# Kernel tuning notes

Hardware: AMD Instinct MI355X
Metric: run time of the kernel (lower is better)

Reference implementation:

```python
import jax, jax.numpy as jnp
import numpy as np

N, L, D = 32, 4096, 768
H = 12
DH = D // H
MLP_DIM = 4 * D


def setup_inputs() -> dict:
    key = jax.random.key(0)
    ks = jax.random.split(key, 12)
    xavier = jax.nn.initializers.xavier_uniform()
    inp = {
        "x": jax.random.normal(ks[0], (N, L, D), jnp.float32),
        "probe": xavier(ks[1], (1, 1, D), jnp.float32),
        # MHA projections (flax DenseGeneral layout: (d, h, dh) / out (h, dh, d))
        "wq": xavier(ks[2], (D, H, DH), jnp.float32),
        "bq": jnp.zeros((H, DH), jnp.float32),
        "wk": xavier(ks[3], (D, H, DH), jnp.float32),
        "bk": jnp.zeros((H, DH), jnp.float32),
        "wv": xavier(ks[4], (D, H, DH), jnp.float32),
        "bv": jnp.zeros((H, DH), jnp.float32),
        "wo": xavier(ks[5], (H, DH, D), jnp.float32),
        "bo": jnp.zeros((D,), jnp.float32),
        # LayerNorm
        "ln_scale": jnp.ones((D,), jnp.float32),
        "ln_bias": jnp.zeros((D,), jnp.float32),
        # MLP block
        "w1": xavier(ks[6], (D, MLP_DIM), jnp.float32),
        "b1": jax.random.normal(ks[7], (MLP_DIM,), jnp.float32) * 1e-6,
        "w2": xavier(ks[8], (MLP_DIM, D), jnp.float32),
        "b2": jax.random.normal(ks[9], (D,), jnp.float32) * 1e-6,
    }
    return inp


def _layernorm(x, scale, bias, eps=1e-6):
    mu = jnp.mean(x, axis=-1, keepdims=True)
    var = jnp.mean(jnp.square(x - mu), axis=-1, keepdims=True)
    return (x - mu) * jax.lax.rsqrt(var + eps) * scale + bias


def reference(x, probe, wq, bq, wk, bk, wv, bv, wo, bo,
              ln_scale, ln_bias, w1, b1, w2, b2):
    n, l, d = x.shape
    q_in = jnp.broadcast_to(probe, (n, 1, d))          # tile probe over batch
    q = jnp.einsum('nqd,dhe->nqhe', q_in, wq) + bq     # [n,1,h,dh]
    k = jnp.einsum('nld,dhe->nlhe', x, wk) + bk        # [n,l,h,dh]
    v = jnp.einsum('nld,dhe->nlhe', x, wv) + bv
    q = q / jnp.sqrt(jnp.asarray(DH, q.dtype))
    logits = jnp.einsum('nqhe,nlhe->nhql', q, k)       # [n,h,1,l]
    attn = jax.nn.softmax(logits, axis=-1)
    o = jnp.einsum('nhql,nlhe->nqhe', attn, v)         # [n,1,h,dh]
    xa = jnp.einsum('nqhe,hed->nqd', o, wo) + bo       # attention output [n,1,d]
    y = _layernorm(xa, ln_scale, ln_bias)
    mlp = jnp.dot(jax.nn.gelu(jnp.dot(y, w1) + b1), w2) + b2
    out = xa + mlp
    return out[:, 0]                                   # [n,d]
```

## Files before the change

### kernel.cpp

```cpp
#include <hip/hip_runtime.h>
#include <math.h>

#define N_B 32
#define L_S 4096
#define D_M 768
#define H_N 12

#define ZO_QH    0
#define ZO_XBAR  1024
#define ZO_O     295936
#define ZO_XA    320512
#define ZO_H1P   345088
#define ZO_MACC  443392
#define ZERO_N   467968
#define NZ_QK    467968
#define NZ_QB    477184
#define NZ_ATTN  477248
#define NZ_Y     2050112
#define NZ_H1    2074688

__global__ __launch_bounds__(256) void qh_kernel(
    const float* __restrict__ probe, const float* __restrict__ wq,
    const float* __restrict__ bq, float* __restrict__ qh) {
    int i = blockIdx.x * 256 + threadIdx.x;
    int d0 = blockIdx.y * 48;
    float acc = 0.f;
    for (int dd = 0; dd < 48; ++dd)
        acc += probe[d0 + dd] * wq[(size_t)(d0 + dd) * 768 + i];
    acc *= 0.125f;
    if (blockIdx.y == 0) acc += 0.125f * bq[i];
    atomicAdd(&qh[i], acc);
}

__global__ __launch_bounds__(256) void qk_kernel(
    const float* __restrict__ qh, const float* __restrict__ wk,
    const float* __restrict__ bk, float* __restrict__ qk,
    float* __restrict__ qb) {
    int h = blockIdx.x, dt = blockIdx.y, t = threadIdx.x;
    int d = dt * 256 + t;
    const float4* wk4 = (const float4*)(wk + (size_t)d * 768 + h * 64);
    const float4* qh4 = (const float4*)(qh + h * 64);
    float acc = 0.f;
    #pragma unroll
    for (int e4 = 0; e4 < 16; ++e4) {
        float4 w = wk4[e4], q = qh4[e4];
        acc += w.x * q.x + w.y * q.y + w.z * q.z + w.w * q.w;
    }
    qk[h * 768 + d] = acc;
    if (dt == 0 && t < 64) {
        float v = qh[h * 64 + t] * bk[h * 64 + t];
        #pragma unroll
        for (int off = 32; off > 0; off >>= 1) v += __shfl_xor(v, off);
        if (t == 0) qb[h] = v;
    }
}

__global__ __launch_bounds__(256) void logits_kernel(
    const float* __restrict__ x, const float* __restrict__ qk,
    const float* __restrict__ qb, float* __restrict__ attn) {
    int r = blockIdx.x * 256 + threadIdx.x;
    int n = r >> 12, l = r & 4095;
    const float4* xr4 = (const float4*)(x + (size_t)r * 768);
    const float4* qk4 = (const float4*)qk;
    float p[12];
    #pragma unroll
    for (int h = 0; h < 12; ++h) p[h] = qb[h];
    for (int d4 = 0; d4 < 192; ++d4) {
        float4 xv = xr4[d4];
        #pragma unroll
        for (int h = 0; h < 12; ++h) {
            float4 qv = qk4[h * 192 + d4];
            p[h] += xv.x * qv.x + xv.y * qv.y + xv.z * qv.z + xv.w * qv.w;
        }
    }
    #pragma unroll
    for (int h = 0; h < 12; ++h)
        attn[((size_t)(n * 12 + h)) * 4096 + l] = p[h];
}

__global__ __launch_bounds__(256) void softmax_kernel(float* __restrict__ attn) {
    float* p = attn + (size_t)blockIdx.x * 4096;
    int tid = threadIdx.x;
    __shared__ float red[4];
    float v[16];
    #pragma unroll
    for (int k = 0; k < 16; ++k) v[k] = p[tid + 256 * k];
    float m = -1e30f;
    #pragma unroll
    for (int k = 0; k < 16; ++k) m = fmaxf(m, v[k]);
    #pragma unroll
    for (int off = 32; off > 0; off >>= 1) m = fmaxf(m, __shfl_xor(m, off));
    int wave = tid >> 6;
    if ((tid & 63) == 0) red[wave] = m;
    __syncthreads();
    m = fmaxf(fmaxf(red[0], red[1]), fmaxf(red[2], red[3]));
    float s = 0.f;
    #pragma unroll
    for (int k = 0; k < 16; ++k) { v[k] = expf(v[k] - m); s += v[k]; }
    #pragma unroll
    for (int off = 32; off > 0; off >>= 1) s += __shfl_xor(s, off);
    __syncthreads();
    if ((tid & 63) == 0) red[wave] = s;
    __syncthreads();
    s = red[0] + red[1] + red[2] + red[3];
    float inv = 1.f / s;
    #pragma unroll
    for (int k = 0; k < 16; ++k) p[tid + 256 * k] = v[k] * inv;
}

__global__ __launch_bounds__(256) void xbar_kernel(
    const float* __restrict__ x, const float* __restrict__ attn,
    float* __restrict__ xbar) {
    int lc = blockIdx.x, dt = blockIdx.y, n = blockIdx.z;
    __shared__ __align__(16) float at_s[512 * 16];
    int t = threadIdx.x;
    for (int i = t; i < 512 * 12; i += 256) {
        int h = i >> 9, l = i & 511;
        at_s[l * 16 + h] = attn[((size_t)(n * 12 + h)) * 4096 + lc * 512 + l];
    }
    __syncthreads();
    int lane = t & 63, w = t >> 6;
    int h0 = w * 3;
    const float4* x4 = (const float4*)x;
    size_t base = ((size_t)n * 4096 + lc * 512) * 192 + dt * 64 + lane;
    float4 a0 = {0, 0, 0, 0}, a1 = {0, 0, 0, 0}, a2 = {0, 0, 0, 0};
    for (int l = 0; l < 512; ++l) {
        float4 xv = x4[base + (size_t)l * 192];
        float w0 = at_s[l * 16 + h0];
        float w1 = at_s[l * 16 + h0 + 1];
        float w2 = at_s[l * 16 + h0 + 2];
        a0.x += w0 * xv.x; a0.y += w0 * xv.y; a0.z += w0 * xv.z; a0.w += w0 * xv.w;
        a1.x += w1 * xv.x; a1.y += w1 * xv.y; a1.z += w1 * xv.z; a1.w += w1 * xv.w;
        a2.x += w2 * xv.x; a2.y += w2 * xv.y; a2.z += w2 * xv.z; a2.w += w2 * xv.w;
    }
    int d = dt * 256 + lane * 4;
    float* b0 = xbar + ((size_t)(n * 12 + h0)) * 768 + d;
    float* b1 = xbar + ((size_t)(n * 12 + h0 + 1)) * 768 + d;
    float* b2 = xbar + ((size_t)(n * 12 + h0 + 2)) * 768 + d;
    atomicAdd(b0 + 0, a0.x); atomicAdd(b0 + 1, a0.y); atomicAdd(b0 + 2, a0.z); atomicAdd(b0 + 3, a0.w);
    atomicAdd(b1 + 0, a1.x); atomicAdd(b1 + 1, a1.y); atomicAdd(b1 + 2, a1.z); atomicAdd(b1 + 3, a1.w);
    atomicAdd(b2 + 0, a2.x); atomicAdd(b2 + 1, a2.y); atomicAdd(b2 + 2, a2.z); atomicAdd(b2 + 3, a2.w);
}

__global__ __launch_bounds__(256) void oproj_kernel(
    const float* __restrict__ xbar, const float* __restrict__ wv,
    const float* __restrict__ bv, float* __restrict__ o) {
    int h = blockIdx.x, kk = blockIdx.y, t = threadIdx.x;
    int d0 = kk * 96;
    __shared__ __align__(16) float wv_s[96 * 64];
    __shared__ __align__(16) float xb_s[96 * 32];
    for (int i = t; i < 96 * 64; i += 256) {
        int d = i >> 6, e = i & 63;
        wv_s[i] = wv[(size_t)(d0 + d) * 768 + h * 64 + e];
    }
    for (int i = t; i < 96 * 32; i += 256) {
        int d = i >> 5, nn = i & 31;
        xb_s[i] = xbar[((size_t)(nn * 12 + h)) * 768 + d0 + d];
    }
    __syncthreads();
    int e = t & 63, ng = t >> 6;
    float acc[8] = {0, 0, 0, 0, 0, 0, 0, 0};
    for (int d = 0; d < 96; ++d) {
        float wvv = wv_s[d * 64 + e];
        const float4* xb4 = (const float4*)&xb_s[d * 32 + ng * 8];
        float4 p0 = xb4[0], p1 = xb4[1];
        acc[0] += p0.x * wvv; acc[1] += p0.y * wvv; acc[2] += p0.z * wvv; acc[3] += p0.w * wvv;
        acc[4] += p1.x * wvv; acc[5] += p1.y * wvv; acc[6] += p1.z * wvv; acc[7] += p1.w * wvv;
    }
    float bvv = (kk == 0) ? bv[h * 64 + e] : 0.f;
    #pragma unroll
    for (int k = 0; k < 8; ++k)
        atomicAdd(&o[(size_t)(ng * 8 + k) * 768 + h * 64 + e], acc[k] + bvv);
}

__global__ __launch_bounds__(256) void xaproj_kernel(
    const float* __restrict__ o, const float* __restrict__ wo,
    const float* __restrict__ bo, float* __restrict__ xa) {
    int dt = blockIdx.x, kk = blockIdx.y, t = threadIdx.x;
    int i0 = kk * 96;
    __shared__ __align__(16) float o_s[96 * 32];
    for (int idx = t; idx < 96 * 32; idx += 256) {
        int i = idx >> 5, nn = idx & 31;
        o_s[idx] = o[(size_t)nn * 768 + i0 + i];
    }
    __syncthreads();
    int d = dt * 256 + t;
    float acc[32];
    #pragma unroll
    for (int nn = 0; nn < 32; ++nn) acc[nn] = 0.f;
    for (int i = 0; i < 96; ++i) {
        float w = wo[(size_t)(i0 + i) * 768 + d];
        const float4* o4 = (const float4*)&o_s[i * 32];
        #pragma unroll
        for (int q = 0; q < 8; ++q) {
            float4 f = o4[q];
            acc[q * 4 + 0] += f.x * w; acc[q * 4 + 1] += f.y * w;
            acc[q * 4 + 2] += f.z * w; acc[q * 4 + 3] += f.w * w;
        }
    }
    float bov = (kk == 0) ? bo[d] : 0.f;
    #pragma unroll
    for (int nn = 0; nn < 32; ++nn)
        atomicAdd(&xa[(size_t)nn * 768 + d], acc[nn] + bov);
}

__global__ __launch_bounds__(256) void ln_kernel(
    const float* __restrict__ xa, const float* __restrict__ ln_scale,
    const float* __restrict__ ln_bias, float* __restrict__ y) {
    int n = blockIdx.x, tid = threadIdx.x;
    __shared__ float xs[768];
    __shared__ float red[4];
    for (int i = tid; i < 768; i += 256) xs[i] = xa[(size_t)n * 768 + i];
    __syncthreads();
    float lsum = 0.f;
    for (int i = tid; i < 768; i += 256) lsum += xs[i];
    #pragma unroll
    for (int off = 32; off > 0; off >>= 1) lsum += __shfl_xor(lsum, off);
    int wave = tid >> 6;
    if ((tid & 63) == 0) red[wave] = lsum;
    __syncthreads();
    float mu = (red[0] + red[1] + red[2] + red[3]) * (1.f / 768.f);
    __syncthreads();
    float lsq = 0.f;
    for (int i = tid; i < 768; i += 256) { float c = xs[i] - mu; lsq += c * c; }
    #pragma unroll
    for (int off = 32; off > 0; off >>= 1) lsq += __shfl_xor(lsq, off);
    if ((tid & 63) == 0) red[wave] = lsq;
    __syncthreads();
    float var = (red[0] + red[1] + red[2] + red[3]) * (1.f / 768.f);
    float rs = rsqrtf(var + 1e-6f);
    for (int i = tid; i < 768; i += 256)
        y[(size_t)n * 768 + i] = (xs[i] - mu) * rs * ln_scale[i] + ln_bias[i];
}

__global__ __launch_bounds__(256) void mlp1_kernel(
    const float* __restrict__ y, const float* __restrict__ w1,
    float* __restrict__ h1p) {
    int jt = blockIdx.x, kk = blockIdx.y, t = threadIdx.x;
    int d0 = kk * 48;
    __shared__ __align__(16) float y_s[48 * 32];
    for (int idx = t; idx < 48 * 32; idx += 256) {
        int d = idx >> 5, nn = idx & 31;
        y_s[idx] = y[(size_t)nn * 768 + d0 + d];
    }
    __syncthreads();
    int j = jt * 256 + t;
    float acc[32];
    #pragma unroll
    for (int nn = 0; nn < 32; ++nn) acc[nn] = 0.f;
    for (int d = 0; d < 48; ++d) {
        float w = w1[(size_t)(d0 + d) * 3072 + j];
        const float4* y4 = (const float4*)&y_s[d * 32];
        #pragma unroll
        for (int q = 0; q < 8; ++q) {
            float4 f = y4[q];
            acc[q * 4 + 0] += f.x * w; acc[q * 4 + 1] += f.y * w;
            acc[q * 4 + 2] += f.z * w; acc[q * 4 + 3] += f.w * w;
        }
    }
    #pragma unroll
    for (int nn = 0; nn < 32; ++nn)
        atomicAdd(&h1p[(size_t)nn * 3072 + j], acc[nn]);
}

__global__ __launch_bounds__(256) void gelu_kernel(
    const float* __restrict__ h1p, const float* __restrict__ b1,
    float* __restrict__ h1) {
    int j = blockIdx.x * 256 + threadIdx.x;
    int n = blockIdx.y;
    float tv = h1p[(size_t)n * 3072 + j] + b1[j];
    float g = 0.5f * tv * (1.f + tanhf(0.7978845608028654f * (tv + 0.044715f * tv * tv * tv)));
    h1[(size_t)n * 3072 + j] = g;
}

__global__ __launch_bounds__(256) void mlp2_kernel(
    const float* __restrict__ h1, const float* __restrict__ w2,
    float* __restrict__ macc) {
    int dt = blockIdx.x, kk = blockIdx.y, t = threadIdx.x;
    int j0 = kk * 48;
    __shared__ __align__(16) float h_s[48 * 32];
    for (int idx = t; idx < 48 * 32; idx += 256) {
        int j = idx >> 5, nn = idx & 31;
        h_s[idx] = h1[(size_t)nn * 3072 + j0 + j];
    }
    __syncthreads();
    int d = dt * 256 + t;
    float acc[32];
    #pragma unroll
    for (int nn = 0; nn < 32; ++nn) acc[nn] = 0.f;
    for (int j = 0; j < 48; ++j) {
        float w = w2[(size_t)(j0 + j) * 768 + d];
        const float4* h4 = (const float4*)&h_s[j * 32];
        #pragma unroll
        for (int q = 0; q < 8; ++q) {
            float4 f = h4[q];
            acc[q * 4 + 0] += f.x * w; acc[q * 4 + 1] += f.y * w;
            acc[q * 4 + 2] += f.z * w; acc[q * 4 + 3] += f.w * w;
        }
    }
    #pragma unroll
    for (int nn = 0; nn < 32; ++nn)
        atomicAdd(&macc[(size_t)nn * 768 + d], acc[nn]);
}

__global__ __launch_bounds__(256) void final_kernel(
    const float* __restrict__ xa, const float* __restrict__ b2,
    const float* __restrict__ macc, float* __restrict__ out) {
    int n = blockIdx.x, t = threadIdx.x;
    for (int i = t; i < 768; i += 256)
        out[(size_t)n * 768 + i] = xa[(size_t)n * 768 + i] + b2[i] + macc[(size_t)n * 768 + i];
}

extern "C" void kernel_launch(void* const* d_in, const int* in_sizes, int n_in,
                              void* d_out, int out_size, void* d_ws, size_t ws_size,
                              hipStream_t stream) {
    const float* x        = (const float*)d_in[0];
    const float* probe    = (const float*)d_in[1];
    const float* wq       = (const float*)d_in[2];
    const float* bq       = (const float*)d_in[3];
    const float* wk       = (const float*)d_in[4];
    const float* bk       = (const float*)d_in[5];
    const float* wv       = (const float*)d_in[6];
    const float* bv       = (const float*)d_in[7];
    const float* wo       = (const float*)d_in[8];
    const float* bo       = (const float*)d_in[9];
    const float* ln_scale = (const float*)d_in[10];
    const float* ln_bias  = (const float*)d_in[11];
    const float* w1       = (const float*)d_in[12];
    const float* b1       = (const float*)d_in[13];
    const float* w2       = (const float*)d_in[14];
    const float* b2       = (const float*)d_in[15];
    float* out = (float*)d_out;
    float* ws  = (float*)d_ws;

    float* qh   = ws + ZO_QH;
    float* xbar = ws + ZO_XBAR;
    float* o    = ws + ZO_O;
    float* xa   = ws + ZO_XA;
    float* h1p  = ws + ZO_H1P;
    float* macc = ws + ZO_MACC;
    float* qk   = ws + NZ_QK;
    float* qb   = ws + NZ_QB;
    float* attn = ws + NZ_ATTN;
    float* y    = ws + NZ_Y;
    float* h1   = ws + NZ_H1;

    hipMemsetAsync(ws, 0, (size_t)ZERO_N * sizeof(float), stream);
    qh_kernel<<<dim3(3, 16), 256, 0, stream>>>(probe, wq, bq, qh);
    qk_kernel<<<dim3(12, 3), 256, 0, stream>>>(qh, wk, bk, qk, qb);
    logits_kernel<<<512, 256, 0, stream>>>(x, qk, qb, attn);
    softmax_kernel<<<N_B * H_N, 256, 0, stream>>>(attn);
    xbar_kernel<<<dim3(8, 3, 32), 256, 0, stream>>>(x, attn, xbar);
    oproj_kernel<<<dim3(12, 8), 256, 0, stream>>>(xbar, wv, bv, o);
    xaproj_kernel<<<dim3(3, 8), 256, 0, stream>>>(o, wo, bo, xa);
    ln_kernel<<<N_B, 256, 0, stream>>>(xa, ln_scale, ln_bias, y);
    mlp1_kernel<<<dim3(12, 16), 256, 0, stream>>>(y, w1, h1p);
    gelu_kernel<<<dim3(12, 32), 256, 0, stream>>>(h1p, b1, h1);
    mlp2_kernel<<<dim3(3, 64), 256, 0, stream>>>(h1, w2, macc);
    final_kernel<<<N_B, 256, 0, stream>>>(xa, b2, macc, out);
}
```

Measured before the change: 820.5 us.

## Coalesce logits via wave-per-row reduction, fuse q/k prep and GELU into neighbours

The logits kernel now assigns one wavefront to each pair of rows. Lanes read contiguous float4 chunks, with qk staged in shared memory, and DPP cross-lane sums replace the old thread-per-row strided access that read whole rows per thread. The two query-prep kernels are merged into one kernel that recomputes qh redundantly in each block. GELU is folded into the mlp2 input load, and xbar reads its attention weights as a float4. These changes target uncoalesced x reads and extra launches, at the cost of redundant qh work in 36 blocks and an extra GELU recompute for each dt block.

```diff
diff --git a/kernel.cpp b/kernel.cpp
--- a/kernel.cpp
+++ b/kernel.cpp
@@ -6,40 +6,48 @@
 #define D_M 768
 #define H_N 12
 
-#define ZO_QH    0
-#define ZO_XBAR  1024
-#define ZO_O     295936
-#define ZO_XA    320512
-#define ZO_H1P   345088
-#define ZO_MACC  443392
-#define ZERO_N   467968
-#define NZ_QK    467968
-#define NZ_QB    477184
-#define NZ_ATTN  477248
-#define NZ_Y     2050112
-#define NZ_H1    2074688
-
-__global__ __launch_bounds__(256) void qh_kernel(
+#define ZO_XBAR  0
+#define ZO_O     294912
+#define ZO_XA    319488
+#define ZO_H1P   344064
+#define ZO_MACC  442368
+#define ZERO_N   466944
+#define NZ_QK    466944
+#define NZ_QB    476160
+#define NZ_ATTN  476224
+#define NZ_Y     2049088
+
+#define DPP_ADD(v, ctrl, rmask) \
+  v += __int_as_float(__builtin_amdgcn_update_dpp(0, __float_as_int(v), ctrl, rmask, 0xf, false))
+
+__device__ __forceinline__ float wave_sum63(float v) {
+    DPP_ADD(v, 0x111, 0xf);
+    DPP_ADD(v, 0x112, 0xf);
+    DPP_ADD(v, 0x114, 0xf);
+    DPP_ADD(v, 0x118, 0xf);
+    DPP_ADD(v, 0x142, 0xa);
+    DPP_ADD(v, 0x143, 0xc);
+    return v;
+}
+
+__global__ __launch_bounds__(256) void prep_kernel(
     const float* __restrict__ probe, const float* __restrict__ wq,
-    const float* __restrict__ bq, float* __restrict__ qh) {
-    int i = blockIdx.x * 256 + threadIdx.x;
-    int d0 = blockIdx.y * 48;
-    float acc = 0.f;
-    for (int dd = 0; dd < 48; ++dd)
-        acc += probe[d0 + dd] * wq[(size_t)(d0 + dd) * 768 + i];
-    acc *= 0.125f;
-    if (blockIdx.y == 0) acc += 0.125f * bq[i];
-    atomicAdd(&qh[i], acc);
-}
-
-__global__ __launch_bounds__(256) void qk_kernel(
-    const float* __restrict__ qh, const float* __restrict__ wk,
+    const float* __restrict__ bq, const float* __restrict__ wk,
     const float* __restrict__ bk, float* __restrict__ qk,
     float* __restrict__ qb) {
     int h = blockIdx.x, dt = blockIdx.y, t = threadIdx.x;
+    __shared__ float qh_s[768];
+    float a0 = bq[t], a1 = bq[t + 256], a2 = bq[t + 512];
+    for (int d = 0; d < 768; ++d) {
+        float p = probe[d];
+        const float* wr = wq + (size_t)d * 768;
+        a0 += p * wr[t]; a1 += p * wr[t + 256]; a2 += p * wr[t + 512];
+    }
+    qh_s[t] = a0 * 0.125f; qh_s[t + 256] = a1 * 0.125f; qh_s[t + 512] = a2 * 0.125f;
+    __syncthreads();
     int d = dt * 256 + t;
     const float4* wk4 = (const float4*)(wk + (size_t)d * 768 + h * 64);
-    const float4* qh4 = (const float4*)(qh + h * 64);
+    const float4* qh4 = (const float4*)(qh_s + h * 64);
     float acc = 0.f;
     #pragma unroll
     for (int e4 = 0; e4 < 16; ++e4) {
@@ -48,34 +56,58 @@
     }
     qk[h * 768 + d] = acc;
     if (dt == 0 && t < 64) {
-        float v = qh[h * 64 + t] * bk[h * 64 + t];
-        #pragma unroll
-        for (int off = 32; off > 0; off >>= 1) v += __shfl_xor(v, off);
-        if (t == 0) qb[h] = v;
-    }
-}
-
-__global__ __launch_bounds__(256) void logits_kernel(
+        float v = qh_s[h * 64 + t] * bk[h * 64 + t];
+        float s = wave_sum63(v);
+        if (t == 63) qb[h] = s;
+    }
+}
+
+__global__ __launch_bounds__(256, 4) void logits_kernel(
     const float* __restrict__ x, const float* __restrict__ qk,
     const float* __restrict__ qb, float* __restrict__ attn) {
-    int r = blockIdx.x * 256 + threadIdx.x;
-    int n = r >> 12, l = r & 4095;
-    const float4* xr4 = (const float4*)(x + (size_t)r * 768);
+    __shared__ float4 qk_s[2304];
+    __shared__ float qb_s[12];
+    int t = threadIdx.x;
     const float4* qk4 = (const float4*)qk;
-    float p[12];
-    #pragma unroll
-    for (int h = 0; h < 12; ++h) p[h] = qb[h];
-    for (int d4 = 0; d4 < 192; ++d4) {
-        float4 xv = xr4[d4];
+    for (int j = t; j < 2304; j += 256) qk_s[j] = qk4[j];
+    if (t < 12) qb_s[t] = qb[t];
+    __syncthreads();
+    int w = t >> 6, lane = t & 63;
+    size_t r0 = ((size_t)blockIdx.x * 4 + w) * 32;
+    for (int rp = 0; rp < 16; ++rp) {
+        size_t rA = r0 + rp * 2, rB = rA + 1;
+        const float4* xA = (const float4*)(x + rA * 768);
+        const float4* xB = (const float4*)(x + rB * 768);
+        float4 a0 = xA[lane], a1 = xA[64 + lane], a2 = xA[128 + lane];
+        float4 b0 = xB[lane], b1 = xB[64 + lane], b2 = xB[128 + lane];
+        float pA[12], pB[12];
         #pragma unroll
         for (int h = 0; h < 12; ++h) {
-            float4 qv = qk4[h * 192 + d4];
-            p[h] += xv.x * qv.x + xv.y * qv.y + xv.z * qv.z + xv.w * qv.w;
-        }
-    }
-    #pragma unroll
-    for (int h = 0; h < 12; ++h)
-        attn[((size_t)(n * 12 + h)) * 4096 + l] = p[h];
+            float4 q0 = qk_s[h * 192 + lane];
+            float4 q1 = qk_s[h * 192 + 64 + lane];
+            float4 q2 = qk_s[h * 192 + 128 + lane];
+            pA[h] = a0.x * q0.x + a0.y * q0.y + a0.z * q0.z + a0.w * q0.w
+                  + a1.x * q1.x + a1.y * q1.y + a1.z * q1.z + a1.w * q1.w
+                  + a2.x * q2.x + a2.y * q2.y + a2.z * q2.z + a2.w * q2.w;
+            pB[h] = b0.x * q0.x + b0.y * q0.y + b0.z * q0.z + b0.w * q0.w
+                  + b1.x * q1.x + b1.y * q1.y + b1.z * q1.z + b1.w * q1.w
+                  + b2.x * q2.x + b2.y * q2.y + b2.z * q2.z + b2.w * q2.w;
+        }
+        #pragma unroll
+        for (int h = 0; h < 12; ++h) {
+            pA[h] = wave_sum63(pA[h]);
+            pB[h] = wave_sum63(pB[h]);
+        }
+        if (lane == 63) {
+            int nA = (int)(rA >> 12), lA = (int)(rA & 4095);
+            int nB = (int)(rB >> 12), lB = (int)(rB & 4095);
+            #pragma unroll
+            for (int h = 0; h < 12; ++h) {
+                attn[((size_t)(nA * 12 + h)) * 4096 + lA] = pA[h] + qb_s[h];
+                attn[((size_t)(nB * 12 + h)) * 4096 + lB] = pB[h] + qb_s[h];
+            }
+        }
+    }
 }
 
 __global__ __launch_bounds__(256) void softmax_kernel(float* __restrict__ attn) {
@@ -114,25 +146,26 @@
     int lc = blockIdx.x, dt = blockIdx.y, n = blockIdx.z;
     __shared__ __align__(16) float at_s[512 * 16];
     int t = threadIdx.x;
-    for (int i = t; i < 512 * 12; i += 256) {
-        int h = i >> 9, l = i & 511;
-        at_s[l * 16 + h] = attn[((size_t)(n * 12 + h)) * 4096 + lc * 512 + l];
+    for (int idx = t; idx < 512 * 12; idx += 256) {
+        int l = idx & 511, hh = idx >> 9;
+        int wg = hh / 3, c = hh - wg * 3;
+        at_s[l * 16 + wg * 4 + c] =
+            attn[((size_t)(n * 12 + hh)) * 4096 + lc * 512 + l];
     }
     __syncthreads();
     int lane = t & 63, w = t >> 6;
-    int h0 = w * 3;
+    const float4* at4 = (const float4*)at_s;
     const float4* x4 = (const float4*)x;
-    size_t base = ((size_t)n * 4096 + lc * 512) * 192 + dt * 64 + lane;
+    size_t base = ((size_t)n * 4096 + (size_t)lc * 512) * 192 + dt * 64 + lane;
     float4 a0 = {0, 0, 0, 0}, a1 = {0, 0, 0, 0}, a2 = {0, 0, 0, 0};
     for (int l = 0; l < 512; ++l) {
         float4 xv = x4[base + (size_t)l * 192];
-        float w0 = at_s[l * 16 + h0];
-        float w1 = at_s[l * 16 + h0 + 1];
-        float w2 = at_s[l * 16 + h0 + 2];
-        a0.x += w0 * xv.x; a0.y += w0 * xv.y; a0.z += w0 * xv.z; a0.w += w0 * xv.w;
-        a1.x += w1 * xv.x; a1.y += w1 * xv.y; a1.z += w1 * xv.z; a1.w += w1 * xv.w;
-        a2.x += w2 * xv.x; a2.y += w2 * xv.y; a2.z += w2 * xv.z; a2.w += w2 * xv.w;
-    }
+        float4 aw = at4[l * 4 + w];
+        a0.x += aw.x * xv.x; a0.y += aw.x * xv.y; a0.z += aw.x * xv.z; a0.w += aw.x * xv.w;
+        a1.x += aw.y * xv.x; a1.y += aw.y * xv.y; a1.z += aw.y * xv.z; a1.w += aw.y * xv.w;
+        a2.x += aw.z * xv.x; a2.y += aw.z * xv.y; a2.z += aw.z * xv.z; a2.w += aw.z * xv.w;
+    }
+    int h0 = w * 3;
     int d = dt * 256 + lane * 4;
     float* b0 = xbar + ((size_t)(n * 12 + h0)) * 768 + d;
     float* b1 = xbar + ((size_t)(n * 12 + h0 + 1)) * 768 + d;
@@ -263,25 +296,17 @@
         atomicAdd(&h1p[(size_t)nn * 3072 + j], acc[nn]);
 }
 
-__global__ __launch_bounds__(256) void gelu_kernel(
+__global__ __launch_bounds__(256) void mlp2_kernel(
     const float* __restrict__ h1p, const float* __restrict__ b1,
-    float* __restrict__ h1) {
-    int j = blockIdx.x * 256 + threadIdx.x;
-    int n = blockIdx.y;
-    float tv = h1p[(size_t)n * 3072 + j] + b1[j];
-    float g = 0.5f * tv * (1.f + tanhf(0.7978845608028654f * (tv + 0.044715f * tv * tv * tv)));
-    h1[(size_t)n * 3072 + j] = g;
-}
-
-__global__ __launch_bounds__(256) void mlp2_kernel(
-    const float* __restrict__ h1, const float* __restrict__ w2,
-    float* __restrict__ macc) {
+    const float* __restrict__ w2, float* __restrict__ macc) {
     int dt = blockIdx.x, kk = blockIdx.y, t = threadIdx.x;
     int j0 = kk * 48;
     __shared__ __align__(16) float h_s[48 * 32];
     for (int idx = t; idx < 48 * 32; idx += 256) {
         int j = idx >> 5, nn = idx & 31;
-        h_s[idx] = h1[(size_t)nn * 3072 + j0 + j];
+        float tv = h1p[(size_t)nn * 3072 + j0 + j] + b1[j0 + j];
+        h_s[idx] = 0.5f * tv * (1.f + tanhf(0.7978845608028654f *
+                       (tv + 0.044715f * tv * tv * tv)));
     }
     __syncthreads();
     int d = dt * 256 + t;
@@ -333,7 +358,6 @@
     float* out = (float*)d_out;
     float* ws  = (float*)d_ws;
 
-    float* qh   = ws + ZO_QH;
     float* xbar = ws + ZO_XBAR;
     float* o    = ws + ZO_O;
     float* xa   = ws + ZO_XA;
@@ -343,19 +367,16 @@
     float* qb   = ws + NZ_QB;
     float* attn = ws + NZ_ATTN;
     float* y    = ws + NZ_Y;
-    float* h1   = ws + NZ_H1;
 
     hipMemsetAsync(ws, 0, (size_t)ZERO_N * sizeof(float), stream);
-    qh_kernel<<<dim3(3, 16), 256, 0, stream>>>(probe, wq, bq, qh);
-    qk_kernel<<<dim3(12, 3), 256, 0, stream>>>(qh, wk, bk, qk, qb);
-    logits_kernel<<<512, 256, 0, stream>>>(x, qk, qb, attn);
+    prep_kernel<<<dim3(12, 3), 256, 0, stream>>>(probe, wq, bq, wk, bk, qk, qb);
+    logits_kernel<<<1024, 256, 0, stream>>>(x, qk, qb, attn);
     softmax_kernel<<<N_B * H_N, 256, 0, stream>>>(attn);
     xbar_kernel<<<dim3(8, 3, 32), 256, 0, stream>>>(x, attn, xbar);
     oproj_kernel<<<dim3(12, 8), 256, 0, stream>>>(xbar, wv, bv, o);
     xaproj_kernel<<<dim3(3, 8), 256, 0, stream>>>(o, wo, bo, xa);
     ln_kernel<<<N_B, 256, 0, stream>>>(xa, ln_scale, ln_bias, y);
     mlp1_kernel<<<dim3(12, 16), 256, 0, stream>>>(y, w1, h1p);
-    gelu_kernel<<<dim3(12, 32), 256, 0, stream>>>(h1p, b1, h1);
-    mlp2_kernel<<<dim3(3, 64), 256, 0, stream>>>(h1, w2, macc);
+    mlp2_kernel<<<dim3(3, 64), 256, 0, stream>>>(h1p, b1, w2, macc);
     final_kernel<<<N_B, 256, 0, stream>>>(xa, b2, macc, out);
 }
```

Result: slower. 1.367 ms (+66.6%).
